# Kernel tuning notes

Hardware: AMD Instinct MI355X
Metric: run time of the kernel (lower is better)

The kernel has to match this reference:

```python
import jax, jax.numpy as jnp
import numpy as np

B, D, W, H = 512, 128, 256, 256  # batch, drive_num, window_size, hidden_size


def setup_inputs() -> dict:
    key = jax.random.key(0)
    k = jax.random.split(key, 7)
    x = jax.random.normal(k[0], (B, D, W), jnp.float32)
    # encode_attn: Linear(window_size + 2*hidden_size, 1)
    attn_w = jax.random.normal(k[1], (W + 2 * H,), jnp.float32) * 0.02
    attn_b = jax.random.normal(k[2], (), jnp.float32) * 0.02
    # single-layer LSTM, input_size=D, hidden_size=H; PyTorch gate order i,f,g,o
    W_ih = jax.random.normal(k[3], (4 * H, D), jnp.float32) * 0.05
    W_hh = jax.random.normal(k[4], (4 * H, H), jnp.float32) * 0.05
    b_ih = jax.random.normal(k[5], (4 * H,), jnp.float32) * 0.05
    b_hh = jax.random.normal(k[6], (4 * H,), jnp.float32) * 0.05
    return {"x": x, "attn_w": attn_w, "attn_b": attn_b,
            "W_ih": W_ih, "W_hh": W_hh, "b_ih": b_ih, "b_hh": b_hh}


def reference(x, attn_w, attn_b, W_ih, W_hh, b_ih, b_hh):
    # x: [B, D, W]
    h_dim = W_hh.shape[1]
    w_h = attn_w[:h_dim]           # weight on repeated hidden state
    w_c = attn_w[h_dim:2 * h_dim]  # weight on repeated cell state
    w_x = attn_w[2 * h_dim:]       # weight on full input row (constant over t)
    # precompute input contribution to attention logits: [B, D]
    e_x = jnp.einsum('bdw,w->bd', x, w_x) + attn_b
    x_steps = jnp.moveaxis(x, 2, 0)  # [W, B, D]

    def step(carry, x_t):
        h, c = carry  # [B, H] each
        # attention logit: h/c terms broadcast over drive dim
        e = e_x + (h @ w_h + c @ w_c)[:, None]  # [B, D]
        a = jax.nn.softmax(e, axis=-1)
        x_hat = a * x_t  # [B, D]
        gates = x_hat @ W_ih.T + b_ih + h @ W_hh.T + b_hh  # [B, 4H]
        i, f, g, o = jnp.split(gates, 4, axis=-1)
        c_new = jax.nn.sigmoid(f) * c + jax.nn.sigmoid(i) * jnp.tanh(g)
        h_new = jax.nn.sigmoid(o) * jnp.tanh(c_new)
        return (h_new, c_new), h_new

    bsz = x.shape[0]
    h0 = jnp.zeros((bsz, h_dim), x.dtype)
    c0 = jnp.zeros((bsz, h_dim), x.dtype)
    _, hs = jax.lax.scan(step, (h0, c0), x_steps)  # hs: [W, B, H]
    return jnp.transpose(hs, (1, 0, 2))  # [B, W, H] == hidden_states[:, 1:]
```

## Files before the change

kernel.cpp:

```cpp
#include <hip/hip_runtime.h>
#include <cstdint>

#define NB 512
#define ND 128
#define NW 256
#define NH 256
#define PGRP 32
#define QGRP 8

typedef _Float16 f16;
typedef _Float16 h8 __attribute__((ext_vector_type(8)));
typedef float f32x4 __attribute__((ext_vector_type(4)));
typedef unsigned long long u64;

#define FLAG_DONE 0x0101010101010101ull

__device__ __forceinline__ float sigm(float v){ return 1.f/(1.f+__expf(-v)); }
__device__ __forceinline__ float tanh_fast(float v){
  v = fminf(fmaxf(v,-15.f),15.f);
  float e = __expf(2.f*v);
  return (e-1.f)/(e+1.f);
}

__global__ __launch_bounds__(128) void attn_kernel(
    const float* __restrict__ x, const float* __restrict__ attn_w,
    const float* __restrict__ attn_b, float* __restrict__ a_buf)
{
    __shared__ float wx[NW];
    __shared__ float sred[2];
    const int b = blockIdx.x;
    const int d = threadIdx.x;

    wx[d]       = attn_w[2 * NH + d];
    wx[d + 128] = attn_w[2 * NH + d + 128];
    __syncthreads();

    const float4* xr = (const float4*)(x + ((size_t)b * ND + d) * NW);
    float acc = 0.f;
    #pragma unroll 8
    for (int w4 = 0; w4 < NW / 4; ++w4) {
        float4 v = xr[w4];
        acc += v.x * wx[w4*4+0] + v.y * wx[w4*4+1]
             + v.z * wx[w4*4+2] + v.w * wx[w4*4+3];
    }
    float e = acc + attn_b[0];

    float mx = e;
    #pragma unroll
    for (int o = 32; o > 0; o >>= 1) mx = fmaxf(mx, __shfl_xor(mx, o));
    if ((d & 63) == 0) sred[d >> 6] = mx;
    __syncthreads();
    mx = fmaxf(sred[0], sred[1]);
    __syncthreads();

    float p = __expf(e - mx);
    float s = p;
    #pragma unroll
    for (int o = 32; o > 0; o >>= 1) s += __shfl_xor(s, o);
    if ((d & 63) == 0) sred[d >> 6] = s;
    __syncthreads();
    s = sred[0] + sred[1];

    a_buf[(size_t)b * ND + d] = p / s;
}

__global__ __launch_bounds__(512) void pack_kernel(
    const float* __restrict__ W_ih, const float* __restrict__ W_hh,
    const float* __restrict__ b_ih, const float* __restrict__ b_hh,
    f16* __restrict__ Wfrag, float* __restrict__ bias)
{
    int flat = blockIdx.x * 512 + threadIdx.x;
    int l    = flat & 63;
    int kt   = (flat >> 6) % 12;
    int wq   = (flat >> 6) / 12;
    int col16 = l & 15, kb = l >> 4;
    int hcol = (wq >> 3) * 32 + (wq & 7) * 4 + (col16 >> 2);
    int gate = col16 & 3;
    int n    = gate * 256 + hcol;
    int k0   = kt * 32 + kb * 8;

    f16 tmp[8];
    #pragma unroll
    for (int e = 0; e < 8; ++e) {
        int k = k0 + e;
        float v = (k < NH) ? W_hh[(size_t)n * NH + k]
                           : W_ih[(size_t)n * ND + (k - NH)];
        tmp[e] = (f16)v;
    }
    *(h8*)(Wfrag + (size_t)flat * 8) = *(const h8*)tmp;

    if (flat < 1024) bias[flat] = b_ih[flat] + b_hh[flat];
}

__global__ __launch_bounds__(512) void init_kernel(unsigned* __restrict__ flags)
{
    flags[blockIdx.x * 512 + threadIdx.x] = 0u;
}

__global__ __launch_bounds__(512, 2) void lstm_kernel(
    const float* __restrict__ x, const float* __restrict__ a_buf,
    const float* __restrict__ bias, const f16* __restrict__ Wfrag,
    f16* __restrict__ hx, u64* __restrict__ flags,
    float* __restrict__ out)
{
    __shared__ __align__(16) unsigned char A16[16 * 768];
    __shared__ float scr[8][272];

    const int tid = threadIdx.x;
    const int w = tid >> 6, l = tid & 63;
    const int p = blockIdx.x & 31, q = blockIdx.x >> 5;

    h8 bfrag[12];
    {
        const h8* wsrc = (const h8*)Wfrag + ((q * 8 + w) * 12) * 64 + l;
        #pragma unroll
        for (int kt = 0; kt < 12; ++kt) bfrag[kt] = wsrc[kt * 64];
    }

    const int m = l >> 2, hh = l & 3;
    const int jcol = q * 32 + w * 4 + hh;
    float bias4[4];
    #pragma unroll
    for (int g = 0; g < 4; ++g) bias4[g] = bias[g * 256 + jcol];
    float cstate = 0.f;

    float areg[8];
    const float* xbase = nullptr;
    const int xrow = tid >> 4, xdc = tid & 15;
    if (tid < 256) {
        int b = p * 16 + xrow;
        #pragma unroll
        for (int e = 0; e < 8; ++e) areg[e] = a_buf[b * ND + xdc * 8 + e];
        xbase = x + ((size_t)b * ND + xdc * 8) * NW;
    }
    const int r2 = tid >> 5, kc = tid & 31;
    const int arow = l & 15, akb = l >> 4;

    float4 xq[8];
    u64 fl_spec = 0;

    {
        int byte = r2 * 768 + kc * 16;
        byte ^= (r2 & 7) << 4;
        h8 z = {};
        *(h8*)(A16 + byte) = z;
    }
    if (tid < 256) {
        #pragma unroll
        for (int e = 0; e < 8; ++e)
            xq[e] = *(const float4*)(xbase + (size_t)e * NW);
        f16 xv[8];
        #pragma unroll
        for (int e = 0; e < 8; ++e) {
            float xf = xq[e].x;
            xq[e] = make_float4(xq[e].y, xq[e].z, xq[e].w, xq[e].x);
            xv[e] = (f16)(xf * areg[e]);
        }
        int byte = xrow * 768 + 512 + xdc * 16;
        byte ^= (xrow & 7) << 4;
        *(h8*)(A16 + byte) = *(const h8*)xv;
    }

    for (int t = 0; t < NW; ++t) {
        if (t > 0 && tid == 0 && fl_spec != FLAG_DONE) {
            while (__hip_atomic_load(&flags[(t - 1) * PGRP + p],
                                     __ATOMIC_RELAXED, __HIP_MEMORY_SCOPE_AGENT)
                   != FLAG_DONE) {}
        }
        __syncthreads();

        f32x4 acc = {0.f, 0.f, 0.f, 0.f};
        if (t > 0) {
            const u64* hrow = (const u64*)
                (hx + ((size_t)((t - 1) & 1) * NB + p * 16 + r2) * NH);
            u64 d0 = __hip_atomic_load(hrow + kc * 2 + 0,
                    __ATOMIC_RELAXED, __HIP_MEMORY_SCOPE_AGENT);
            u64 d1 = __hip_atomic_load(hrow + kc * 2 + 1,
                    __ATOMIC_RELAXED, __HIP_MEMORY_SCOPE_AGENT);
            #pragma unroll
            for (int kt = 8; kt < 12; ++kt) {
                int byte = arow * 768 + kt * 64 + akb * 16;
                byte ^= (arow & 7) << 4;
                h8 afrag = *(const h8*)(A16 + byte);
                acc = __builtin_amdgcn_mfma_f32_16x16x32_f16(afrag, bfrag[kt], acc, 0, 0, 0);
            }
            int byte = r2 * 768 + kc * 16;
            byte ^= (r2 & 7) << 4;
            ((u64*)(A16 + byte))[0] = d0;
            ((u64*)(A16 + byte))[1] = d1;
        } else {
            #pragma unroll
            for (int kt = 8; kt < 12; ++kt) {
                int byte = arow * 768 + kt * 64 + akb * 16;
                byte ^= (arow & 7) << 4;
                h8 afrag = *(const h8*)(A16 + byte);
                acc = __builtin_amdgcn_mfma_f32_16x16x32_f16(afrag, bfrag[kt], acc, 0, 0, 0);
            }
        }
        __syncthreads();

        #pragma unroll
        for (int kt = 0; kt < 8; ++kt) {
            int byte = arow * 768 + kt * 64 + akb * 16;
            byte ^= (arow & 7) << 4;
            h8 afrag = *(const h8*)(A16 + byte);
            acc = __builtin_amdgcn_mfma_f32_16x16x32_f16(afrag, bfrag[kt], acc, 0, 0, 0);
        }

        float hn;
        {
            float* sw = &scr[w][0];
            int col = l & 15, rb = (l >> 4) * 4;
            sw[(rb + 0) * 17 + col] = acc[0];
            sw[(rb + 1) * 17 + col] = acc[1];
            sw[(rb + 2) * 17 + col] = acc[2];
            sw[(rb + 3) * 17 + col] = acc[3];
            asm volatile("s_waitcnt lgkmcnt(0)" ::: "memory");
            float G0 = sw[m * 17 + hh * 4 + 0] + bias4[0];
            float G1 = sw[m * 17 + hh * 4 + 1] + bias4[1];
            float G2 = sw[m * 17 + hh * 4 + 2] + bias4[2];
            float G3 = sw[m * 17 + hh * 4 + 3] + bias4[3];
            float ig = sigm(G0), fg = sigm(G1);
            float gg = tanh_fast(G2), og = sigm(G3);
            cstate = fg * cstate + ig * gg;
            hn = og * tanh_fast(cstate);

            f16 hf = (f16)hn;
            unsigned short hb = __builtin_bit_cast(unsigned short, hf);
            int other = __shfl_xor((int)hb, 1);
            if (!(l & 1)) {
                unsigned val = (unsigned)hb | ((unsigned)(unsigned short)other << 16);
                unsigned* dst = (unsigned*)((unsigned short*)hx
                                + ((size_t)(t & 1) * NB + p * 16 + m) * NH + jcol);
                __hip_atomic_store(dst, val, __ATOMIC_RELAXED, __HIP_MEMORY_SCOPE_AGENT);
            }
        }
        asm volatile("s_waitcnt vmcnt(0)" ::: "memory");
        __syncthreads();

        if (tid == 0 && t < NW - 1) {
            unsigned char* fb = ((unsigned char*)&flags[t * PGRP + p]) + q;
            __hip_atomic_store(fb, (unsigned char)1,
                               __ATOMIC_RELAXED, __HIP_MEMORY_SCOPE_AGENT);
        }

        out[((size_t)(p * 16 + m) * NW + t) * NH + jcol] = hn;

        if (tid < 256 && t + 1 < NW) {
            if (((t + 1) & 3) == 0) {
                #pragma unroll
                for (int e = 0; e < 8; ++e)
                    xq[e] = *(const float4*)(xbase + (size_t)e * NW + (t + 1));
            }
            f16 xv[8];
            #pragma unroll
            for (int e = 0; e < 8; ++e) {
                float xf = xq[e].x;
                xq[e] = make_float4(xq[e].y, xq[e].z, xq[e].w, xq[e].x);
                xv[e] = (f16)(xf * areg[e]);
            }
            int byte = xrow * 768 + 512 + xdc * 16;
            byte ^= (xrow & 7) << 4;
            *(h8*)(A16 + byte) = *(const h8*)xv;
        }

        if (tid == 0 && t < NW - 1) {
            fl_spec = __hip_atomic_load(&flags[t * PGRP + p],
                                        __ATOMIC_RELAXED, __HIP_MEMORY_SCOPE_AGENT);
        }
    }
}

extern "C" void kernel_launch(void* const* d_in, const int* in_sizes, int n_in,
                              void* d_out, int out_size, void* d_ws, size_t ws_size,
                              hipStream_t stream) {
    (void)in_sizes; (void)n_in; (void)out_size;

    const float* x      = (const float*)d_in[0];
    const float* attn_w = (const float*)d_in[1];
    const float* attn_b = (const float*)d_in[2];
    const float* W_ih   = (const float*)d_in[3];
    const float* W_hh   = (const float*)d_in[4];
    const float* b_ih   = (const float*)d_in[5];
    const float* b_hh   = (const float*)d_in[6];
    float* out = (float*)d_out;

    char* ws = (char*)d_ws;
    float* a_buf = (float*)ws;
    float* bias  = (float*)(ws + 262144);
    f16*   Wfrag = (f16*)(ws + 266240);
    f16*   hx    = (f16*)(ws + 1052672);
    u64*   flags = (u64*)(ws + 1576960);
    if (ws_size < (size_t)1642496) return;

    attn_kernel<<<NB, 128, 0, stream>>>(x, attn_w, attn_b, a_buf);
    pack_kernel<<<96, 512, 0, stream>>>(W_ih, W_hh, b_ih, b_hh, Wfrag, bias);
    init_kernel<<<32, 512, 0, stream>>>((unsigned*)flags);
    lstm_kernel<<<PGRP * QGRP, 512, 0, stream>>>(x, a_buf, bias, Wfrag, hx, flags, out);
}
```

Measured before the change: 762.2 us.

## Keep own hidden-state chunk in LDS and poll step flag earlier

Each block now writes its own slice of the new hidden state straight into its shared-memory A tile. It does that MFMA chunk before the barrier, and it no longer reloads that slice from the global hx buffer. This shortens the part of the recurrent matmul that has to wait for other blocks' flags and removes one eighth of the cross-block global loads. A second speculative poll of the step flag is added earlier in the iteration, so the spin-wait can be skipped more often. The cost is extra branching and one more flag load per step.

```diff
diff --git a/kernel.cpp b/kernel.cpp
--- a/kernel.cpp
+++ b/kernel.cpp
@@ -134,10 +134,11 @@
         xbase = x + ((size_t)b * ND + xdc * 8) * NW;
     }
     const int r2 = tid >> 5, kc = tid & 31;
+    const bool ownchunk = ((kc >> 2) == q);
     const int arow = l & 15, akb = l >> 4;
 
     float4 xq[8];
-    u64 fl_spec = 0;
+    u64 fl_spec1 = 0, fl_spec2 = 0;
 
     {
         int byte = r2 * 768 + kc * 16;
@@ -162,7 +163,8 @@
     }
 
     for (int t = 0; t < NW; ++t) {
-        if (t > 0 && tid == 0 && fl_spec != FLAG_DONE) {
+        if (t > 0 && tid == 0 &&
+            fl_spec1 != FLAG_DONE && fl_spec2 != FLAG_DONE) {
             while (__hip_atomic_load(&flags[(t - 1) * PGRP + p],
                                      __ATOMIC_RELAXED, __HIP_MEMORY_SCOPE_AGENT)
                    != FLAG_DONE) {}
@@ -171,12 +173,15 @@
 
         f32x4 acc = {0.f, 0.f, 0.f, 0.f};
         if (t > 0) {
+            u64 d0 = 0, d1 = 0;
             const u64* hrow = (const u64*)
                 (hx + ((size_t)((t - 1) & 1) * NB + p * 16 + r2) * NH);
-            u64 d0 = __hip_atomic_load(hrow + kc * 2 + 0,
-                    __ATOMIC_RELAXED, __HIP_MEMORY_SCOPE_AGENT);
-            u64 d1 = __hip_atomic_load(hrow + kc * 2 + 1,
-                    __ATOMIC_RELAXED, __HIP_MEMORY_SCOPE_AGENT);
+            if (!ownchunk) {
+                d0 = __hip_atomic_load(hrow + kc * 2 + 0,
+                        __ATOMIC_RELAXED, __HIP_MEMORY_SCOPE_AGENT);
+                d1 = __hip_atomic_load(hrow + kc * 2 + 1,
+                        __ATOMIC_RELAXED, __HIP_MEMORY_SCOPE_AGENT);
+            }
             #pragma unroll
             for (int kt = 8; kt < 12; ++kt) {
                 int byte = arow * 768 + kt * 64 + akb * 16;
@@ -184,10 +189,18 @@
                 h8 afrag = *(const h8*)(A16 + byte);
                 acc = __builtin_amdgcn_mfma_f32_16x16x32_f16(afrag, bfrag[kt], acc, 0, 0, 0);
             }
-            int byte = r2 * 768 + kc * 16;
-            byte ^= (r2 & 7) << 4;
-            ((u64*)(A16 + byte))[0] = d0;
-            ((u64*)(A16 + byte))[1] = d1;
+            {
+                int byte = arow * 768 + q * 64 + akb * 16;
+                byte ^= (arow & 7) << 4;
+                h8 afrag = *(const h8*)(A16 + byte);
+                acc = __builtin_amdgcn_mfma_f32_16x16x32_f16(afrag, bfrag[q], acc, 0, 0, 0);
+            }
+            if (!ownchunk) {
+                int byte = r2 * 768 + kc * 16;
+                byte ^= (r2 & 7) << 4;
+                ((u64*)(A16 + byte))[0] = d0;
+                ((u64*)(A16 + byte))[1] = d1;
+            }
         } else {
             #pragma unroll
             for (int kt = 8; kt < 12; ++kt) {
@@ -196,11 +209,18 @@
                 h8 afrag = *(const h8*)(A16 + byte);
                 acc = __builtin_amdgcn_mfma_f32_16x16x32_f16(afrag, bfrag[kt], acc, 0, 0, 0);
             }
+            {
+                int byte = arow * 768 + q * 64 + akb * 16;
+                byte ^= (arow & 7) << 4;
+                h8 afrag = *(const h8*)(A16 + byte);
+                acc = __builtin_amdgcn_mfma_f32_16x16x32_f16(afrag, bfrag[q], acc, 0, 0, 0);
+            }
         }
         __syncthreads();
 
         #pragma unroll
         for (int kt = 0; kt < 8; ++kt) {
+            if (kt == q) continue;
             int byte = arow * 768 + kt * 64 + akb * 16;
             byte ^= (arow & 7) << 4;
             h8 afrag = *(const h8*)(A16 + byte);
@@ -226,6 +246,11 @@
             hn = og * tanh_fast(cstate);
 
             f16 hf = (f16)hn;
+            {
+                int bown = m * 768 + jcol * 2;
+                bown ^= (m & 7) << 4;
+                *(f16*)(A16 + bown) = hf;
+            }
             unsigned short hb = __builtin_bit_cast(unsigned short, hf);
             int other = __shfl_xor((int)hb, 1);
             if (!(l & 1)) {
@@ -246,6 +271,11 @@
 
         out[((size_t)(p * 16 + m) * NW + t) * NH + jcol] = hn;
 
+        if (tid == 0 && t < NW - 1) {
+            fl_spec1 = __hip_atomic_load(&flags[t * PGRP + p],
+                                         __ATOMIC_RELAXED, __HIP_MEMORY_SCOPE_AGENT);
+        }
+
         if (tid < 256 && t + 1 < NW) {
             if (((t + 1) & 3) == 0) {
                 #pragma unroll
@@ -265,8 +295,8 @@
         }
 
         if (tid == 0 && t < NW - 1) {
-            fl_spec = __hip_atomic_load(&flags[t * PGRP + p],
-                                        __ATOMIC_RELAXED, __HIP_MEMORY_SCOPE_AGENT);
+            fl_spec2 = __hip_atomic_load(&flags[t * PGRP + p],
+                                         __ATOMIC_RELAXED, __HIP_MEMORY_SCOPE_AGENT);
         }
     }
 }
```

Result: slower. 875.5 us (+14.9%).
